# Optimization experiments

Hardware: AMD Instinct MI355X
Metric: run time of the kernel (lower is better)

The kernel has to match this reference:

```python
import jax, jax.numpy as jnp
import numpy as np

STRIDES = (8, 16, 32)
IMG = 640
REG_MAX = 16
TOPK = 10
ALPHA = 0.5
BETA = 6.0
EPS_IOU = 1e-16


def _make_anchors():
    # anchor centers for all pyramid levels, (N, 2) in pixel coords
    pts = []
    for s in STRIDES:
        h = w = IMG // s
        ys, xs = jnp.meshgrid(jnp.arange(h, dtype=jnp.float32),
                              jnp.arange(w, dtype=jnp.float32), indexing='ij')
        a = (jnp.stack([xs, ys], axis=-1).reshape(-1, 2) + 0.5) * s
        pts.append(a)
    return jnp.concatenate(pts, axis=0)  # (8400, 2)


def _iou_pairwise(pred, gt):
    # pred (B,N,4), gt (B,M,4) -> IoU (B,M,N)
    b1 = pred[:, None, :, :]   # (B,1,N,4)
    b2 = gt[:, :, None, :]     # (B,M,1,4)
    tl = jnp.maximum(b1[..., :2], b2[..., :2])
    br = jnp.minimum(b1[..., 2:], b2[..., 2:])
    wh = jnp.clip(br - tl, 0.0)
    inter = wh[..., 0] * wh[..., 1]
    a1 = (b1[..., 2] - b1[..., 0]) * (b1[..., 3] - b1[..., 1])
    a2 = (b2[..., 2] - b2[..., 0]) * (b2[..., 3] - b2[..., 1])
    return inter / (a1 + a2 - inter + EPS_IOU)


def _iou_1v1(b1, b2):
    # elementwise IoU, both (..., 4)
    tl = jnp.maximum(b1[..., :2], b2[..., :2])
    br = jnp.minimum(b1[..., 2:], b2[..., 2:])
    wh = jnp.clip(br - tl, 0.0)
    inter = wh[..., 0] * wh[..., 1]
    a1 = (b1[..., 2] - b1[..., 0]) * (b1[..., 3] - b1[..., 1])
    a2 = (b2[..., 2] - b2[..., 0]) * (b2[..., 3] - b2[..., 1])
    return inter / (a1 + a2 - inter + EPS_IOU)


def setup_inputs() -> dict:
    key = jax.random.key(0)
    ks = jax.random.split(key, 6)
    B, N, NC, M = 32, 8400, 80, 40
    pred_scores = jax.random.normal(ks[0], (B, N, NC), jnp.float32)
    pred_dist = jax.random.normal(ks[1], (B, N, 4 * REG_MAX), jnp.float32)
    gt_labels = jax.random.randint(ks[2], (B, M, 1), 0, NC, dtype=jnp.int32)
    cxy = jax.random.uniform(ks[3], (B, M, 2), jnp.float32) * 560.0 + 40.0
    wh = jax.random.uniform(ks[4], (B, M, 2), jnp.float32) * 120.0 + 20.0
    gt_bboxes = jnp.concatenate([jnp.clip(cxy - wh / 2, 0.0, float(IMG)),
                                 jnp.clip(cxy + wh / 2, 0.0, float(IMG))], axis=-1)
    dfl_weight = jax.random.normal(ks[5], (REG_MAX,), jnp.float32) * 0.05
    return {"pred_scores": pred_scores, "pred_dist": pred_dist,
            "gt_labels": gt_labels, "gt_bboxes": gt_bboxes,
            "dfl_weight": dfl_weight}


def reference(pred_scores, pred_dist, gt_labels, gt_bboxes, dfl_weight):
    B, N, NC = pred_scores.shape
    M = gt_bboxes.shape[1]
    anchors = _make_anchors()  # (N, 2)

    # DFL: softmax over reg bins, weighted sum with (random-init) conv weight
    prob = jax.nn.softmax(pred_dist.reshape(B, N, 4, REG_MAX), axis=-1)
    ltrb = prob @ dfl_weight                      # (B,N,4)
    pred_bboxes = jnp.concatenate([anchors - ltrb[..., :2],
                                   anchors + ltrb[..., 2:]], axis=-1)  # (B,N,4) xyxy

    # ---- task-aligned assigner (no-grad) ----
    sg = jax.lax.stop_gradient
    sig = jax.nn.sigmoid(sg(pred_scores))         # (B,N,NC)
    labels = gt_labels[..., 0].astype(jnp.int32)  # (B,M)
    sigT = jnp.swapaxes(sig, 1, 2)                # (B,NC,N)
    scores = jnp.take_along_axis(sigT, jnp.broadcast_to(labels[:, :, None], (B, M, N)), axis=1)  # (B,M,N)
    ious = jnp.clip(_iou_pairwise(sg(pred_bboxes), gt_bboxes), 0.0)      # (B,M,N)
    align = scores ** ALPHA * ious ** BETA        # (B,M,N)

    _, topk_idxs = jax.lax.top_k(align, TOPK)     # (B,M,TOPK) over anchors
    mask = jnp.zeros((B * M, N), dtype=align.dtype)
    mask = mask.at[jnp.arange(B * M)[:, None], topk_idxs.reshape(B * M, TOPK)].set(1.0)
    mask = mask.reshape(B, M, N)
    mask = mask * (align > 1e-9).astype(align.dtype)
    max_m = align.max(axis=1)                     # (B,N) best metric per anchor
    mask = mask * (align == max_m[:, None, :]).astype(align.dtype)

    fg_mask = mask.max(axis=1)                    # (B,N) in {0,1}
    tgt_idx = mask.argmax(axis=1)                 # (B,N) assigned gt index
    ts_sum = jnp.maximum(fg_mask.sum(), 1.0)

    # ---- classification targets (vectorized scatter) ----
    asg_labels = jnp.take_along_axis(labels, tgt_idx, axis=1)  # (B,N)
    target_scores = jax.nn.one_hot(asg_labels, NC, dtype=pred_scores.dtype) * (max_m * fg_mask)[..., None]

    x = pred_scores
    bce = jnp.maximum(x, 0.0) - x * target_scores + jnp.log1p(jnp.exp(-jnp.abs(x)))
    loss_cls = bce.sum() / ts_sum

    # ---- box IoU loss on positives (vectorized gather + mask) ----
    gt_asg = jnp.take_along_axis(gt_bboxes, tgt_idx[..., None], axis=1)  # (B,N,4)
    iou1 = _iou_1v1(pred_bboxes, gt_asg)          # (B,N)
    fg = fg_mask.sum()
    loss_box = jnp.where(fg > 0, ((1.0 - iou1) * fg_mask).sum() / fg, 0.0)

    return loss_cls + loss_box * 1.5
```

## Files before the change

kernel.cpp:

```cpp
#include <hip/hip_runtime.h>
#include <cstdint>
#include <cstddef>

#define BB 32
#define NN 8400
#define NCC 80
#define MM 40
#define RM 16
#define TOPKK 10
#define CAP 2048
#define SLOTP 41

__device__ __forceinline__ void anchor_xy(int n, float& ax, float& ay) {
    int s, x, y;
    if (n < 6400)      { s = 8;  y = n / 80;            x = n - y * 80; }
    else if (n < 8000) { int i = n - 6400; s = 16; y = i / 40; x = i - y * 40; }
    else               { int i = n - 8000; s = 32; y = i / 20; x = i - y * 20; }
    ax = ((float)x + 0.5f) * (float)s;
    ay = ((float)y + 0.5f) * (float)s;
}

__global__ __launch_bounds__(256) void k_main(const float* __restrict__ ps,
                                              const float* __restrict__ pd,
                                              const int*   __restrict__ gl,
                                              const float* __restrict__ gb,
                                              const float* __restrict__ w,
                                              float* __restrict__ pbb,
                                              float* __restrict__ maxm,
                                              int*   __restrict__ cnts,
                                              unsigned long long* __restrict__ lists,
                                              float* __restrict__ accum,
                                              int*   __restrict__ tgt) {
    __shared__ float  sc[128 * SLOTP];
    __shared__ float4 box[128];
    __shared__ float  gtb[MM * 4];
    __shared__ int    glab[MM];
    __shared__ int    slotm[MM];
    __shared__ int    cmap[NCC];
    __shared__ float  cm[256];
    __shared__ float  redf[4];
    const int b  = blockIdx.y;
    const int n0 = blockIdx.x * 128;
    const int t  = threadIdx.x;

    if (t < 128 && n0 + t < NN) tgt[(size_t)b * NN + n0 + t] = 0x7F7F7F7F;

    if (t < MM * 4)              gtb[t] = gb[b * MM * 4 + t];
    if (t >= 192 && t < 192+MM)  glab[t - 192] = gl[b * MM + (t - 192)];
    if (t >= 64 && t < 64+NCC)   cmap[t - 64] = 0x7FFFFFFF;
    __syncthreads();
    if (t < MM) atomicMin(&cmap[glab[t]], t);
    __syncthreads();

    float4 xa[8];
    #pragma unroll
    for (int h = 0; h < 2; h++) {
        int f = t + h * 256;
        int a = f >> 2, side = f & 3;
        int nc = min(n0 + a, NN - 1);
        const float* p = pd + (((size_t)(b * NN + nc)) * 4 + side) * RM;
        #pragma unroll
        for (int i = 0; i < 4; i++) xa[h * 4 + i] = *(const float4*)(p + i * 4);
    }
    float4 vv[10];
    #pragma unroll
    for (int k = 0; k < 10; k++) {
        int f = t + k * 256;
        int row = f / 20, c4 = f - row * 20;
        int nc = min(n0 + row, NN - 1);
        vv[k] = *(const float4*)(ps + ((size_t)(b * NN + nc)) * NCC + c4 * 4);
    }

    if (t < MM) slotm[t] = cmap[glab[t]];

    #pragma unroll
    for (int h = 0; h < 2; h++) {
        int f = t + h * 256;
        float x[RM];
        #pragma unroll
        for (int i = 0; i < 4; i++) {
            float4 v = xa[h * 4 + i];
            x[i*4+0] = v.x; x[i*4+1] = v.y; x[i*4+2] = v.z; x[i*4+3] = v.w;
        }
        float mx = x[0];
        #pragma unroll
        for (int i = 1; i < RM; i++) mx = fmaxf(mx, x[i]);
        float s = 0.f, d = 0.f;
        #pragma unroll
        for (int i = 0; i < RM; i++) {
            float e = __builtin_amdgcn_exp2f((x[i] - mx) * 1.44269504f);
            s += e; d += e * w[i];
        }
        ((float*)box)[f] = d * __builtin_amdgcn_rcpf(s);
    }
    __syncthreads();
    if (t < 128) {
        int n = n0 + t;
        float ax, ay; anchor_xy(min(n, NN - 1), ax, ay);
        float4 v = box[t];
        float4 pb = make_float4(ax - v.x, ay - v.y, ax + v.z, ay + v.w);
        box[t] = pb;
        if (n < NN) *(float4*)(pbb + (size_t)(b * NN + n) * 4) = pb;
    }

    float sp = 0.f;
    #pragma unroll
    for (int k = 0; k < 10; k++) {
        int f = t + k * 256;
        int row = f / 20, c4 = f - row * 20;
        float vmask = (n0 + row < NN) ? 1.f : 0.f;
        float xs[4] = {vv[k].x, vv[k].y, vv[k].z, vv[k].w};
        #pragma unroll
        for (int j = 0; j < 4; j++) {
            float x = xs[j];
            float e = __builtin_amdgcn_exp2f(-1.44269504f * fabsf(x));
            float r = __builtin_amdgcn_rcpf(1.0f + e);
            sp += vmask * (fmaxf(x, 0.f) + 0.69314718f * __builtin_amdgcn_logf(1.0f + e));
            int sl = cmap[c4 * 4 + j];
            if (sl < MM) sc[row * SLOTP + sl] = (x >= 0.f) ? r : e * r;
        }
    }
    __syncthreads();

    const int nloc = t & 127;
    const int n    = n0 + nloc;
    const int mb   = (t >> 7) * 20;
    const int lane = t & 63;
    const bool valid = (n < NN);
    float cmax = -INFINITY;
    float4 p4 = box[nloc];
    const float px1 = p4.x, py1 = p4.y, px2 = p4.z, py2 = p4.w;
    const float a1 = (px2 - px1) * (py2 - py1);
    #pragma unroll
    for (int j = 0; j < 20; j++) {
        int m = mb + j;
        float gx1 = gtb[m*4+0], gy1 = gtb[m*4+1], gx2 = gtb[m*4+2], gy2 = gtb[m*4+3];
        float a2 = (gx2 - gx1) * (gy2 - gy1);
        float iw = fmaxf(fminf(px2, gx2) - fmaxf(px1, gx1), 0.f);
        float ih = fmaxf(fminf(py2, gy2) - fmaxf(py1, gy1), 0.f);
        float inter = iw * ih;
        float iou = fmaxf(inter * __builtin_amdgcn_rcpf(a1 + a2 - inter + 1e-16f), 0.f);
        float al = 0.f;
        if (valid) {
            float sg = sc[nloc * SLOTP + slotm[m]];
            float i2 = iou * iou;
            al = __builtin_amdgcn_sqrtf(sg) * (i2 * i2 * i2);
        }
        cmax = fmaxf(cmax, al);
        bool pos = valid && (al > 1e-9f);
        unsigned long long msk = __ballot(pos);
        if (msk) {
            int leader = __ffsll((long long)msk) - 1;
            int basev = 0;
            if (lane == leader) basev = atomicAdd(&cnts[b * MM + m], __popcll(msk));
            basev = __shfl(basev, leader);
            if (pos) {
                int ofs = __popcll(msk & ((1ull << lane) - 1ull));
                int idx = basev + ofs;
                if (idx < CAP)
                    lists[((size_t)(b * MM + m)) * CAP + idx] =
                        ((unsigned long long)__float_as_uint(al) << 32) | (unsigned)n;
            }
        }
    }
    cm[t] = cmax;
    __syncthreads();
    if (t < 128 && valid) maxm[(size_t)b * NN + n] = fmaxf(cm[t], cm[t + 128]);

    #pragma unroll
    for (int off = 32; off > 0; off >>= 1) sp += __shfl_down(sp, off);
    if ((t & 63) == 0) redf[t >> 6] = sp;
    __syncthreads();
    if (t == 0) atomicAdd(accum, redf[0] + redf[1] + redf[2] + redf[3]);
}

__global__ __launch_bounds__(64) void k_topk(const unsigned long long* __restrict__ lists,
                                             const int*   __restrict__ cnts,
                                             const float* __restrict__ maxm,
                                             int* __restrict__ tgt) {
    __shared__ unsigned long long keys[CAP];
    __shared__ unsigned long long sel[TOPKK];
    const int bm = blockIdx.x, b = bm / MM, m = bm % MM, t = threadIdx.x;
    int cnt = min(cnts[bm], CAP);
    int kk = min(TOPKK, cnt);
    for (int i = t; i < cnt; i += 64) {
        unsigned long long L = lists[(size_t)bm * CAP + i];
        keys[i] = (L & 0xFFFFFFFF00000000ull) | (0xFFFFFFFFull - (L & 0xFFFFFFFFull));
    }
    __syncthreads();
    for (int p = 0; p < kk; p++) {
        unsigned long long best = 0ull;
        for (int i = t; i < cnt; i += 64) best = keys[i] > best ? keys[i] : best;
        #pragma unroll
        for (int off = 32; off > 0; off >>= 1) {
            unsigned long long o = __shfl_xor(best, off);
            best = o > best ? o : best;
        }
        for (int i = t; i < cnt; i += 64) if (keys[i] == best) keys[i] = 0ull;
        if (t == 0) sel[p] = best;
        __syncthreads();
    }
    if (t < kk) {
        unsigned long long bb = sel[t];
        float v = __uint_as_float((unsigned)(bb >> 32));
        int n = (int)(0xFFFFFFFFull - (bb & 0xFFFFFFFFull));
        if (v == maxm[(size_t)b * NN + n]) atomicMin(&tgt[(size_t)b * NN + n], m);
    }
}

__global__ __launch_bounds__(256) void k_fg(const int*   __restrict__ tgt,
                                            const int*   __restrict__ gl,
                                            const float* __restrict__ gb,
                                            const float* __restrict__ ps,
                                            const float* __restrict__ pbb,
                                            const float* __restrict__ maxm,
                                            float* __restrict__ accum) {
    int i = blockIdx.x * 256 + threadIdx.x;
    int t = threadIdx.x;
    float vdot = 0.f, vbox = 0.f, vfg = 0.f;
    int tg = tgt[i];
    if (tg < MM) {
        int b = i / NN;
        int lab = gl[b * MM + tg];
        float x = ps[(size_t)i * NCC + lab];
        float mm = maxm[i];
        float4 p = *(const float4*)(pbb + (size_t)i * 4);
        const float* g = gb + ((size_t)b * MM + tg) * 4;
        float a1 = (p.z - p.x) * (p.w - p.y);
        float a2 = (g[2] - g[0]) * (g[3] - g[1]);
        float iw = fmaxf(fminf(p.z, g[2]) - fmaxf(p.x, g[0]), 0.f);
        float ih = fmaxf(fminf(p.w, g[3]) - fmaxf(p.y, g[1]), 0.f);
        float inter = iw * ih;
        float iou = inter / (a1 + a2 - inter + 1e-16f);
        vdot = x * mm; vbox = 1.0f - iou; vfg = 1.0f;
    }
    #pragma unroll
    for (int off = 32; off > 0; off >>= 1) {
        vdot += __shfl_down(vdot, off);
        vbox += __shfl_down(vbox, off);
        vfg  += __shfl_down(vfg,  off);
    }
    __shared__ float r[3][4];
    if ((t & 63) == 0) { int wv = t >> 6; r[0][wv] = vdot; r[1][wv] = vbox; r[2][wv] = vfg; }
    __syncthreads();
    if (t < 3) {
        float s = r[t][0] + r[t][1] + r[t][2] + r[t][3];
        if (s != 0.f) atomicAdd(&accum[1 + t], s);
    }
}

__global__ void k_final(const float* __restrict__ accum, float* __restrict__ out) {
    float S0 = accum[0], dot = accum[1], box = accum[2], fg = accum[3];
    float ts = fmaxf(fg, 1.0f);
    float cls = (S0 - dot) / ts;
    float lb = (fg > 0.f) ? box / fg : 0.f;
    out[0] = cls + 1.5f * lb;
}

extern "C" void kernel_launch(void* const* d_in, const int* in_sizes, int n_in,
                              void* d_out, int out_size, void* d_ws, size_t ws_size,
                              hipStream_t stream) {
    const float* ps = (const float*)d_in[0];
    const float* pd = (const float*)d_in[1];
    const int*   gl = (const int*)  d_in[2];
    const float* gb = (const float*)d_in[3];
    const float* w  = (const float*)d_in[4];

    char* ws = (char*)d_ws;
    constexpr size_t ACC_BYTES  = 256;
    constexpr size_t CNT_BYTES  = 8192;
    constexpr size_t PBB_BYTES  = (size_t)BB * NN * 4 * sizeof(float);
    constexpr size_t MAXM_BYTES = (size_t)BB * NN * sizeof(float);
    constexpr size_t TGT_BYTES  = (size_t)BB * NN * sizeof(int);

    float* accum = (float*)ws;
    int*   cnts  = (int*)  (ws + ACC_BYTES);
    float* pbb   = (float*)(ws + ACC_BYTES + CNT_BYTES);
    float* maxm  = (float*)(ws + ACC_BYTES + CNT_BYTES + PBB_BYTES);
    int*   tgt   = (int*)  (ws + ACC_BYTES + CNT_BYTES + PBB_BYTES + MAXM_BYTES);
    unsigned long long* lists =
        (unsigned long long*)(ws + ACC_BYTES + CNT_BYTES + PBB_BYTES + MAXM_BYTES + TGT_BYTES);

    hipMemsetAsync(ws, 0, ACC_BYTES + CNT_BYTES, stream);

    dim3 g3((NN + 127) / 128, BB);
    k_main<<<g3, 256, 0, stream>>>(ps, pd, gl, gb, w, pbb, maxm, cnts, lists, accum, tgt);
    k_topk<<<BB * MM, 64, 0, stream>>>(lists, cnts, maxm, tgt);
    k_fg<<<BB * NN / 256, 256, 0, stream>>>(tgt, gl, gb, ps, pbb, maxm, accum);
    k_final<<<1, 1, 0, stream>>>(accum, (float*)d_out);
}
```

Baseline: 194.3 us.

## Split fused main kernel into DFL decode and alignment kernels with smaller anchor tiles

Measured after the change: 224.8 us. 1.16x slower.

```diff
diff --git a/kernel.cpp b/kernel.cpp
--- a/kernel.cpp
+++ b/kernel.cpp
@@ -10,6 +10,7 @@
 #define TOPKK 10
 #define CAP 2048
 #define SLOTP 41
+#define AB 64
 
 __device__ __forceinline__ void anchor_xy(int n, float& ax, float& ay) {
     int s, x, y;
@@ -20,19 +21,56 @@
     ay = ((float)y + 0.5f) * (float)s;
 }
 
-__global__ __launch_bounds__(256) void k_main(const float* __restrict__ ps,
-                                              const float* __restrict__ pd,
-                                              const int*   __restrict__ gl,
-                                              const float* __restrict__ gb,
-                                              const float* __restrict__ w,
-                                              float* __restrict__ pbb,
-                                              float* __restrict__ maxm,
-                                              int*   __restrict__ cnts,
-                                              unsigned long long* __restrict__ lists,
-                                              float* __restrict__ accum,
-                                              int*   __restrict__ tgt) {
-    __shared__ float  sc[128 * SLOTP];
-    __shared__ float4 box[128];
+__global__ __launch_bounds__(256) void k_dfl(const float* __restrict__ pd,
+                                             const float* __restrict__ w,
+                                             float* __restrict__ pbb,
+                                             int*   __restrict__ tgt) {
+    const int b  = blockIdx.y;
+    const int n0 = blockIdx.x * 128;
+    const int t  = threadIdx.x;
+
+    if (t < 128 && n0 + t < NN) tgt[(size_t)b * NN + n0 + t] = 0x7F7F7F7F;
+
+    #pragma unroll
+    for (int h = 0; h < 2; h++) {
+        int f = t + h * 256;
+        int a = f >> 2, side = f & 3;
+        int n = n0 + a;
+        int nc = min(n, NN - 1);
+        const float* p = pd + (((size_t)(b * NN + nc)) * 4 + side) * RM;
+        float x[RM];
+        #pragma unroll
+        for (int i = 0; i < 4; i++) {
+            float4 v = *(const float4*)(p + i * 4);
+            x[i*4+0] = v.x; x[i*4+1] = v.y; x[i*4+2] = v.z; x[i*4+3] = v.w;
+        }
+        float mx = x[0];
+        #pragma unroll
+        for (int i = 1; i < RM; i++) mx = fmaxf(mx, x[i]);
+        float s = 0.f, d = 0.f;
+        #pragma unroll
+        for (int i = 0; i < RM; i++) {
+            float e = __builtin_amdgcn_exp2f((x[i] - mx) * 1.44269504f);
+            s += e; d += e * w[i];
+        }
+        d *= __builtin_amdgcn_rcpf(s);
+        float ax, ay; anchor_xy(nc, ax, ay);
+        float axy = (side & 1) ? ay : ax;
+        float v = (side < 2) ? (axy - d) : (axy + d);
+        if (n < NN) pbb[((size_t)(b * NN + n)) * 4 + side] = v;
+    }
+}
+
+__global__ __launch_bounds__(256) void k_align(const float* __restrict__ ps,
+                                               const int*   __restrict__ gl,
+                                               const float* __restrict__ gb,
+                                               const float* __restrict__ pbb,
+                                               float* __restrict__ maxm,
+                                               int*   __restrict__ cnts,
+                                               unsigned long long* __restrict__ lists,
+                                               float* __restrict__ accum) {
+    __shared__ float  sc[AB * SLOTP];
+    __shared__ float4 box[AB];
     __shared__ float  gtb[MM * 4];
     __shared__ int    glab[MM];
     __shared__ int    slotm[MM];
@@ -40,72 +78,32 @@
     __shared__ float  cm[256];
     __shared__ float  redf[4];
     const int b  = blockIdx.y;
-    const int n0 = blockIdx.x * 128;
+    const int n0 = blockIdx.x * AB;
     const int t  = threadIdx.x;
-
-    if (t < 128 && n0 + t < NN) tgt[(size_t)b * NN + n0 + t] = 0x7F7F7F7F;
 
     if (t < MM * 4)              gtb[t] = gb[b * MM * 4 + t];
     if (t >= 192 && t < 192+MM)  glab[t - 192] = gl[b * MM + (t - 192)];
-    if (t >= 64 && t < 64+NCC)   cmap[t - 64] = 0x7FFFFFFF;
+    if (t >= 96 && t < 96+NCC)   cmap[t - 96] = 0x7FFFFFFF;
+    if (t < AB) {
+        int nc = min(n0 + t, NN - 1);
+        box[t] = *(const float4*)(pbb + ((size_t)(b * NN + nc)) * 4);
+    }
     __syncthreads();
     if (t < MM) atomicMin(&cmap[glab[t]], t);
     __syncthreads();
-
-    float4 xa[8];
-    #pragma unroll
-    for (int h = 0; h < 2; h++) {
-        int f = t + h * 256;
-        int a = f >> 2, side = f & 3;
-        int nc = min(n0 + a, NN - 1);
-        const float* p = pd + (((size_t)(b * NN + nc)) * 4 + side) * RM;
-        #pragma unroll
-        for (int i = 0; i < 4; i++) xa[h * 4 + i] = *(const float4*)(p + i * 4);
-    }
-    float4 vv[10];
-    #pragma unroll
-    for (int k = 0; k < 10; k++) {
+    if (t < MM) slotm[t] = cmap[glab[t]];
+
+    float4 vv[5];
+    #pragma unroll
+    for (int k = 0; k < 5; k++) {
         int f = t + k * 256;
         int row = f / 20, c4 = f - row * 20;
         int nc = min(n0 + row, NN - 1);
         vv[k] = *(const float4*)(ps + ((size_t)(b * NN + nc)) * NCC + c4 * 4);
     }
-
-    if (t < MM) slotm[t] = cmap[glab[t]];
-
-    #pragma unroll
-    for (int h = 0; h < 2; h++) {
-        int f = t + h * 256;
-        float x[RM];
-        #pragma unroll
-        for (int i = 0; i < 4; i++) {
-            float4 v = xa[h * 4 + i];
-            x[i*4+0] = v.x; x[i*4+1] = v.y; x[i*4+2] = v.z; x[i*4+3] = v.w;
-        }
-        float mx = x[0];
-        #pragma unroll
-        for (int i = 1; i < RM; i++) mx = fmaxf(mx, x[i]);
-        float s = 0.f, d = 0.f;
-        #pragma unroll
-        for (int i = 0; i < RM; i++) {
-            float e = __builtin_amdgcn_exp2f((x[i] - mx) * 1.44269504f);
-            s += e; d += e * w[i];
-        }
-        ((float*)box)[f] = d * __builtin_amdgcn_rcpf(s);
-    }
-    __syncthreads();
-    if (t < 128) {
-        int n = n0 + t;
-        float ax, ay; anchor_xy(min(n, NN - 1), ax, ay);
-        float4 v = box[t];
-        float4 pb = make_float4(ax - v.x, ay - v.y, ax + v.z, ay + v.w);
-        box[t] = pb;
-        if (n < NN) *(float4*)(pbb + (size_t)(b * NN + n) * 4) = pb;
-    }
-
     float sp = 0.f;
     #pragma unroll
-    for (int k = 0; k < 10; k++) {
+    for (int k = 0; k < 5; k++) {
         int f = t + k * 256;
         int row = f / 20, c4 = f - row * 20;
         float vmask = (n0 + row < NN) ? 1.f : 0.f;
@@ -122,9 +120,9 @@
     }
     __syncthreads();
 
-    const int nloc = t & 127;
+    const int nloc = t & 63;
     const int n    = n0 + nloc;
-    const int mb   = (t >> 7) * 20;
+    const int mb   = (t >> 6) * 10;
     const int lane = t & 63;
     const bool valid = (n < NN);
     float cmax = -INFINITY;
@@ -132,7 +130,7 @@
     const float px1 = p4.x, py1 = p4.y, px2 = p4.z, py2 = p4.w;
     const float a1 = (px2 - px1) * (py2 - py1);
     #pragma unroll
-    for (int j = 0; j < 20; j++) {
+    for (int j = 0; j < 10; j++) {
         int m = mb + j;
         float gx1 = gtb[m*4+0], gy1 = gtb[m*4+1], gx2 = gtb[m*4+2], gy2 = gtb[m*4+3];
         float a2 = (gx2 - gx1) * (gy2 - gy1);
@@ -165,7 +163,9 @@
     }
     cm[t] = cmax;
     __syncthreads();
-    if (t < 128 && valid) maxm[(size_t)b * NN + n] = fmaxf(cm[t], cm[t + 128]);
+    if (t < AB && valid)
+        maxm[(size_t)b * NN + n] =
+            fmaxf(fmaxf(cm[t], cm[t + 64]), fmaxf(cm[t + 128], cm[t + 192]));
 
     #pragma unroll
     for (int off = 32; off > 0; off >>= 1) sp += __shfl_down(sp, off);
@@ -283,8 +283,10 @@
 
     hipMemsetAsync(ws, 0, ACC_BYTES + CNT_BYTES, stream);
 
-    dim3 g3((NN + 127) / 128, BB);
-    k_main<<<g3, 256, 0, stream>>>(ps, pd, gl, gb, w, pbb, maxm, cnts, lists, accum, tgt);
+    dim3 gdfl((NN + 127) / 128, BB);
+    k_dfl<<<gdfl, 256, 0, stream>>>(pd, w, pbb, tgt);
+    dim3 gal((NN + AB - 1) / AB, BB);
+    k_align<<<gal, 256, 0, stream>>>(ps, gl, gb, pbb, maxm, cnts, lists, accum);
     k_topk<<<BB * MM, 64, 0, stream>>>(lists, cnts, maxm, tgt);
     k_fg<<<BB * NN / 256, 256, 0, stream>>>(tgt, gl, gb, ps, pbb, maxm, accum);
     k_final<<<1, 1, 0, stream>>>(accum, (float*)d_out);
```
